# Optimization experiments

Measured on AMD Instinct MI355X. Metric: run time of the kernel, lower is better.

## Reference

```python
import jax, jax.numpy as jnp
import numpy as np

D = 2048
N = 16384
E = 8
THRESHOLD = 0.5


def setup_inputs() -> dict:
    key = jax.random.key(0)
    ks = jax.random.split(key, 6)
    x = jax.random.normal(ks[0], (N, D), dtype=jnp.float32)
    # pretrained weight + truncated SVD basis (frozen in original module)
    W_np = np.asarray(jax.random.normal(ks[1], (D, D), dtype=jnp.float32))
    U, S, Vt = np.linalg.svd(W_np, full_matrices=False)
    k = int((np.cumsum(S) < THRESHOLD * S.sum()).sum())  # energy-threshold rank
    U_k = jnp.asarray(U[:, :k])
    V_k = jnp.asarray(Vt.T[:, :k])  # torch.svd returns V, not V^T
    W = jnp.asarray(W_np)
    lambda_k = jax.random.normal(ks[2], (E, k), dtype=jnp.float32)
    v = jnp.zeros((D,), dtype=jnp.float32)
    W_g1 = jax.random.normal(ks[3], (k, 1), dtype=jnp.float32)
    W_g2 = jax.random.normal(ks[4], (1, E), dtype=jnp.float32)
    return {"x": x, "W": W, "U_k": U_k, "V_k": V_k, "lambda_k": lambda_k,
            "v": v, "W_g1": W_g1, "W_g2": W_g2}


def reference(x, W, U_k, V_k, lambda_k, v, W_g1, W_g2):
    # Routing: g = softmax((x @ U_k) @ W_g1 @ W_g2)  -> [N, E]
    xu = x @ U_k                                   # [N, k] (shared with delta path)
    g = jax.nn.softmax((xu @ W_g1) @ W_g2, axis=-1)
    # sum_i g_i * (x @ (W + U diag(lam_i) V^T))
    #   = (x@W) * sum_i g_i  +  ((x@U) * (g @ lam)) @ V^T   (low-rank factored)
    base = x @ W                                   # [N, D], computed once
    coef = g @ lambda_k                            # [N, k]
    out = base * jnp.sum(g, axis=-1, keepdims=True) + (xu * coef) @ V_k.T
    return out * (1.0 + v)
```

## Files before the change

### kernel.cpp

```cpp
#include <hip/hip_runtime.h>
#include <hip/hip_bf16.h>

#define D_DIM 2048
#define E_DIM 8

typedef __attribute__((ext_vector_type(8))) short short8;
typedef __attribute__((ext_vector_type(4))) float f32x4;

__device__ __forceinline__ unsigned short f2bf(float f) {
  union { float f; unsigned int u; } v; v.f = f;
  unsigned int u = v.u;
  u += 0x7FFFu + ((u >> 16) & 1u);
  return (unsigned short)(u >> 16);
}

__device__ __forceinline__ void async_copy16(const void* g, void* l) {
  __builtin_amdgcn_global_load_lds((const __attribute__((address_space(1))) void*)g,
                                   (__attribute__((address_space(3))) void*)l,
                                   16, 0, 0);
}

__global__ void k_transpose_bf16(const float* __restrict__ in, int in_rows, int in_cols,
                                 int in_ld, unsigned short* __restrict__ out, int out_rows) {
  __shared__ float tile[32][33];
  const int tx = threadIdx.x;
  const int ty = threadIdx.y;
  const int c = blockIdx.x * 32 + tx;
  #pragma unroll
  for (int i = 0; i < 4; ++i) {
    const int r = blockIdx.y * 32 + ty + i * 8;
    float vv = 0.0f;
    if (r < in_rows && c < in_cols) vv = in[(size_t)r * in_ld + c];
    tile[ty + i * 8][tx] = vv;
  }
  __syncthreads();
  const int oc = blockIdx.y * 32 + tx;
  #pragma unroll
  for (int i = 0; i < 4; ++i) {
    const int orow = blockIdx.x * 32 + ty + i * 8;
    if (orow < out_rows && oc < in_rows)
      out[(size_t)orow * in_rows + oc] = f2bf(tile[tx][ty + i * 8]);
  }
}

__global__ void k_pad_bf16(const float* __restrict__ in, unsigned short* __restrict__ out,
                           int rows, int cols, int cols_pad) {
  long long idx = (long long)blockIdx.x * blockDim.x + threadIdx.x;
  const long long total = (long long)rows * cols_pad;
  const long long stride = (long long)gridDim.x * blockDim.x;
  for (; idx < total; idx += stride) {
    const int r = (int)(idx / cols_pad);
    const int c = (int)(idx % cols_pad);
    out[idx] = (c < cols) ? f2bf(in[(size_t)r * cols + c]) : (unsigned short)0;
  }
}

__global__ void k_u1(const float* __restrict__ U, const float* __restrict__ Wg1,
                     float* __restrict__ u1, int D, int k) {
  const int w = threadIdx.x >> 6;
  const int lane = threadIdx.x & 63;
  const int d = blockIdx.x * 4 + w;
  if (d >= D) return;
  const float* row = U + (size_t)d * k;
  float s = 0.0f;
  for (int j = lane; j < k; j += 64) s += row[j] * Wg1[j];
  #pragma unroll
  for (int off = 32; off; off >>= 1) s += __shfl_xor(s, off);
  if (lane == 0) u1[d] = s;
}

__global__ void k_cvtgate(const float* __restrict__ x,
                          unsigned short* __restrict__ xb,
                          const float* __restrict__ u1, const float* __restrict__ Wg2,
                          float* __restrict__ g8, int Nrows) {
  const int w = threadIdx.x >> 6;
  const int lane = threadIdx.x & 63;
  const int row = blockIdx.x * 4 + w;
  if (row >= Nrows) return;
  const float* xr = x + (size_t)row * D_DIM;
  unsigned short* xo = xb + (size_t)row * D_DIM;
  float s = 0.0f;
  #pragma unroll
  for (int t = 0; t < D_DIM / 512; ++t) {
    const int base = (t * 64 + lane) * 8;
    float4 a = *(const float4*)(xr + base);
    float4 b = *(const float4*)(xr + base + 4);
    float4 ua = *(const float4*)(u1 + base);
    float4 ub = *(const float4*)(u1 + base + 4);
    s += a.x * ua.x + a.y * ua.y + a.z * ua.z + a.w * ua.w +
         b.x * ub.x + b.y * ub.y + b.z * ub.z + b.w * ub.w;
    short8 r;
    r[0] = (short)f2bf(a.x); r[1] = (short)f2bf(a.y);
    r[2] = (short)f2bf(a.z); r[3] = (short)f2bf(a.w);
    r[4] = (short)f2bf(b.x); r[5] = (short)f2bf(b.y);
    r[6] = (short)f2bf(b.z); r[7] = (short)f2bf(b.w);
    *(short8*)(xo + base) = r;
  }
  #pragma unroll
  for (int off = 32; off; off >>= 1) s += __shfl_xor(s, off);
  if (lane == 0) {
    float lg[E_DIM], mx = -INFINITY;
    #pragma unroll
    for (int e = 0; e < E_DIM; ++e) { lg[e] = s * Wg2[e]; mx = fmaxf(mx, lg[e]); }
    float Z = 0.0f;
    #pragma unroll
    for (int e = 0; e < E_DIM; ++e) { lg[e] = expf(lg[e] - mx); Z += lg[e]; }
    const float inv = 1.0f / Z;
    #pragma unroll
    for (int e = 0; e < E_DIM; ++e) g8[(size_t)row * E_DIM + e] = lg[e] * inv;
  }
}

__global__ __launch_bounds__(256, 3) void k_gemm128(
    const unsigned short* __restrict__ A, long long lda,
    const unsigned short* __restrict__ B, long long ldb,
    int Ktot,
    const float* __restrict__ g8, const float* __restrict__ lam, int k_real,
    unsigned short* __restrict__ A2, int lda2) {
  __shared__ unsigned short lds[2 * 8192];
  const int tid = threadIdx.x;
  const int lane = tid & 63;
  const int w = tid >> 6;
  const long long brow = (long long)blockIdx.x * 128;
  const long long bcol = (long long)blockIdx.y * 128;
  const int c0 = w * 2;
  const int sr0 = lane >> 2;
  const int sj  = lane & 3;
  const int l15 = lane & 15;
  const int jhi = lane >> 4;
  const int wr = (w >> 1) * 64;
  const int wc = (w & 1) * 64;

  auto stage = [&](int tt) {
    unsigned short* dstA = lds + (tt & 1) * 8192;
    #pragma unroll
    for (int c = 0; c < 2; ++c) {
      const int chunk = c0 + c;
      const int lrow = chunk * 16 + sr0;
      const int jj = sj ^ ((lrow >> 1) & 3);
      async_copy16(A + (brow + lrow) * lda + (long long)tt * 32 + jj * 8,
                   (void*)(dstA + chunk * 512));
      async_copy16(B + (bcol + lrow) * ldb + (long long)tt * 32 + jj * 8,
                   (void*)(dstA + 4096 + chunk * 512));
    }
  };

  f32x4 acc[4][4];
  #pragma unroll
  for (int m = 0; m < 4; ++m)
    #pragma unroll
    for (int n = 0; n < 4; ++n)
      #pragma unroll
      for (int j = 0; j < 4; ++j) acc[m][n][j] = 0.0f;

  const int NT = Ktot >> 5;
  stage(0);
  asm volatile("s_waitcnt vmcnt(0)" ::: "memory");
  __builtin_amdgcn_s_barrier();

  for (int t = 0; t < NT; ++t) {
    const unsigned short* Areg = lds + (t & 1) * 8192;
    const unsigned short* Breg = Areg + 4096;
    if (t + 1 < NT) stage(t + 1);
    short8 av[4], bv[4];
    #pragma unroll
    for (int m = 0; m < 4; ++m) {
      const int row = wr + m * 16 + l15;
      const int jj = jhi ^ ((row >> 1) & 3);
      av[m] = *(const short8*)(Areg + row * 32 + jj * 8);
    }
    #pragma unroll
    for (int n = 0; n < 4; ++n) {
      const int row = wc + n * 16 + l15;
      const int jj = jhi ^ ((row >> 1) & 3);
      bv[n] = *(const short8*)(Breg + row * 32 + jj * 8);
    }
    __builtin_amdgcn_s_setprio(1);
    #pragma unroll
    for (int m = 0; m < 4; ++m)
      #pragma unroll
      for (int n = 0; n < 4; ++n)
        acc[m][n] = __builtin_amdgcn_mfma_f32_16x16x32_bf16(av[m], bv[n], acc[m][n], 0, 0, 0);
    __builtin_amdgcn_s_setprio(0);
    asm volatile("s_waitcnt vmcnt(0)" ::: "memory");
    __builtin_amdgcn_s_barrier();
  }

  float lamE[E_DIM][4];
  #pragma unroll
  for (int n = 0; n < 4; ++n) {
    const long long col = bcol + wc + n * 16 + l15;
    #pragma unroll
    for (int e = 0; e < E_DIM; ++e)
      lamE[e][n] = (col < k_real) ? lam[(size_t)e * k_real + col] : 0.0f;
  }
  #pragma unroll
  for (int m = 0; m < 4; ++m) {
    float coef[4][4];
    #pragma unroll
    for (int j = 0; j < 4; ++j)
      #pragma unroll
      for (int n = 0; n < 4; ++n) coef[j][n] = 0.0f;
    #pragma unroll
    for (int j = 0; j < 4; ++j) {
      const long long row = brow + wr + m * 16 + jhi * 4 + j;
      const float* gr = g8 + row * E_DIM;
      #pragma unroll
      for (int e = 0; e < E_DIM; ++e) {
        const float ge = gr[e];
        #pragma unroll
        for (int n = 0; n < 4; ++n) coef[j][n] += ge * lamE[e][n];
      }
    }
    #pragma unroll
    for (int n = 0; n < 4; ++n) {
      const long long col = bcol + wc + n * 16 + l15;
      #pragma unroll
      for (int j = 0; j < 4; ++j) {
        const long long row = brow + wr + m * 16 + jhi * 4 + j;
        A2[row * lda2 + col] = f2bf(acc[m][n][j] * coef[j][n]);
      }
    }
  }
}

template<int EPI>
__global__ __launch_bounds__(512, 2) void k_gemm256(
    const unsigned short* __restrict__ A0, int lda0,
    const unsigned short* __restrict__ A1, int lda1,
    const unsigned short* __restrict__ B0, int ldb0,
    const unsigned short* __restrict__ B1, int ldb1,
    int ka0, int Ktot, int gridM,
    float* __restrict__ Cout, int ldc,
    const float* __restrict__ vcol) {
  __shared__ unsigned short lds[4 * 16384];
  const int tid = threadIdx.x;
  const int lane = tid & 63;
  const int w = tid >> 6;
  const int wm = w >> 2;
  const int wn = w & 3;

  int bid = blockIdx.x;
  const int cpx = gridDim.x >> 3;
  bid = (bid & 7) * cpx + (bid >> 3);
  const int bx = bid % gridM;
  const int by = bid / gridM;
  const long long brow = (long long)bx * 256;
  const long long bcol = (long long)by * 256;

  const int c0 = w * 2;
  const int sr0 = lane >> 2;
  const int sj  = lane & 3;
  const int l15 = lane & 15;
  const int jhi = lane >> 4;

  auto stage = [&](int tt) {
    const int k0 = tt * 32;
    const unsigned short* PA; long long ldA; long long kA;
    const unsigned short* PB; long long ldB; long long kB;
    if (k0 < ka0) { PA = A0; ldA = lda0; kA = k0;       PB = B0; ldB = ldb0; kB = k0; }
    else          { PA = A1; ldA = lda1; kA = k0 - ka0; PB = B1; ldB = ldb1; kB = k0 - ka0; }
    unsigned short* dst = lds + (tt & 3) * 16384;
    #pragma unroll
    for (int c = 0; c < 2; ++c) {
      const int chunk = c0 + c;
      const int lrow = chunk * 16 + sr0;
      const int jj = sj ^ ((lrow >> 1) & 3);
      async_copy16(PA + (brow + lrow) * ldA + kA + jj * 8, (void*)(dst + chunk * 512));
      async_copy16(PB + (bcol + lrow) * ldB + kB + jj * 8, (void*)(dst + 8192 + chunk * 512));
    }
  };

  auto load_frags = [&](int tt, short8* av, short8* bv) {
    const unsigned short* Areg = lds + (tt & 3) * 16384;
    const unsigned short* Breg = Areg + 8192;
    #pragma unroll
    for (int m = 0; m < 8; ++m) {
      const int row = wm * 128 + m * 16 + l15;
      const int jj = jhi ^ ((row >> 1) & 3);
      av[m] = *(const short8*)(Areg + row * 32 + jj * 8);
    }
    #pragma unroll
    for (int n = 0; n < 4; ++n) {
      const int row = wn * 64 + n * 16 + l15;
      const int jj = jhi ^ ((row >> 1) & 3);
      bv[n] = *(const short8*)(Breg + row * 32 + jj * 8);
    }
  };

  f32x4 acc[8][4];
  #pragma unroll
  for (int m = 0; m < 8; ++m)
    #pragma unroll
    for (int n = 0; n < 4; ++n)
      #pragma unroll
      for (int j = 0; j < 4; ++j) acc[m][n][j] = 0.0f;

  auto do_mfma = [&](short8* av, short8* bv) {
    __builtin_amdgcn_s_setprio(1);
    #pragma unroll
    for (int m = 0; m < 8; ++m)
      #pragma unroll
      for (int n = 0; n < 4; ++n)
        acc[m][n] = __builtin_amdgcn_mfma_f32_16x16x32_bf16(av[m], bv[n], acc[m][n], 0, 0, 0);
    __builtin_amdgcn_s_setprio(0);
  };

  const int NT = Ktot >> 5;
  stage(0); stage(1); stage(2);
  asm volatile("s_waitcnt vmcnt(4)" ::: "memory");
  __builtin_amdgcn_s_barrier();

  short8 avA[8], bvA[4], avB[8], bvB[4];
  load_frags(0, avA, bvA);

  for (int t = 0; t < NT; t += 2) {
    if (t + 3 < NT) stage(t + 3);
    load_frags(t + 1, avB, bvB);
    do_mfma(avA, bvA);
    asm volatile("s_waitcnt vmcnt(4)" ::: "memory");
    __builtin_amdgcn_s_barrier();
    if (t + 4 < NT) stage(t + 4);
    if (t + 2 < NT) load_frags(t + 2, avA, bvA);
    do_mfma(avB, bvB);
    asm volatile("s_waitcnt vmcnt(4)" ::: "memory");
    __builtin_amdgcn_s_barrier();
  }

  #pragma unroll
  for (int m = 0; m < 8; ++m) {
    #pragma unroll
    for (int n = 0; n < 4; ++n) {
      const long long col = bcol + wn * 64 + n * 16 + l15;
      float cs = 1.0f;
      if (EPI == 1) cs = 1.0f + vcol[col];
      #pragma unroll
      for (int j = 0; j < 4; ++j) {
        const long long row = brow + wm * 128 + m * 16 + jhi * 4 + j;
        Cout[row * ldc + col] = acc[m][n][j] * cs;
      }
    }
  }
}

extern "C" void kernel_launch(void* const* d_in, const int* in_sizes, int n_in,
                              void* d_out, int out_size, void* d_ws, size_t ws_size,
                              hipStream_t stream) {
  const float* x   = (const float*)d_in[0];
  const float* W   = (const float*)d_in[1];
  const float* U   = (const float*)d_in[2];
  const float* V   = (const float*)d_in[3];
  const float* lam = (const float*)d_in[4];
  const float* v   = (const float*)d_in[5];
  const float* Wg1 = (const float*)d_in[6];
  const float* Wg2 = (const float*)d_in[7];
  float* out = (float*)d_out;

  const int N = in_sizes[0] / D_DIM;
  const int k = in_sizes[2] / D_DIM;
  const int k_pad = (k + 127) & ~127;

  char* ws = (char*)d_ws;
  size_t off = 0;
  auto alloc = [&](size_t bytes) -> void* {
    void* p = ws + off;
    off += (bytes + 255) & ~(size_t)255;
    return p;
  };
  unsigned short* xb  = (unsigned short*)alloc((size_t)N * D_DIM * 2);
  unsigned short* Wt  = (unsigned short*)alloc((size_t)D_DIM * D_DIM * 2);
  unsigned short* Ukt = (unsigned short*)alloc((size_t)k_pad * D_DIM * 2);
  unsigned short* Vb  = (unsigned short*)alloc((size_t)D_DIM * k_pad * 2);
  unsigned short* A2  = (unsigned short*)alloc((size_t)N * k_pad * 2);
  float*          u1  = (float*)alloc((size_t)D_DIM * 4);
  float*          g8  = (float*)alloc((size_t)N * E_DIM * 4);
  if (off > ws_size) return;

  k_u1<<<D_DIM / 4, 256, 0, stream>>>(U, Wg1, u1, D_DIM, k);
  k_cvtgate<<<N / 4, 256, 0, stream>>>(x, xb, u1, Wg2, g8, N);
  k_transpose_bf16<<<dim3(D_DIM / 32, D_DIM / 32), dim3(32, 8), 0, stream>>>(
      W, D_DIM, D_DIM, D_DIM, Wt, D_DIM);
  k_transpose_bf16<<<dim3(k_pad / 32, D_DIM / 32), dim3(32, 8), 0, stream>>>(
      U, D_DIM, k, k, Ukt, k_pad);
  k_pad_bf16<<<512, 256, 0, stream>>>(V, Vb, D_DIM, k, k_pad);

  k_gemm128<<<dim3(N / 128, k_pad / 128), 256, 0, stream>>>(
      xb, D_DIM, Ukt, D_DIM, D_DIM, g8, lam, k, A2, k_pad);

  const int gridM = N / 256;
  const int gridN = D_DIM / 256;
  k_gemm256<1><<<gridM * gridN, 512, 0, stream>>>(
      xb, D_DIM, A2, k_pad,
      Wt, D_DIM, Vb, k_pad,
      D_DIM, D_DIM + k_pad, gridM,
      out, D_DIM, v);
}
```

Baseline: 311.1 us.

## Restructure 256x256 GEMM mainloop into K=64 double-buffered, quarter-wise staged pipeline

Replaces the four-stage K=32 LDS ring with a two-buffer K=64 layout. Each iteration is split into four MFMA quarters, and the async loads for the next tile's A and B halves are interleaved between those quarters. The LDS swizzle changes to an XOR over 8-element chunks per 64-wide row, and fragment reads are reused across sub-blocks to cut register pressure. The aim is finer overlap of global-to-LDS traffic with MFMA work. The cost is more barriers per iteration and subtle correctness risk in the buffer-reuse ordering.

```diff
diff --git a/kernel.cpp b/kernel.cpp
--- a/kernel.cpp
+++ b/kernel.cpp
@@ -233,7 +233,7 @@
     int ka0, int Ktot, int gridM,
     float* __restrict__ Cout, int ldc,
     const float* __restrict__ vcol) {
-  __shared__ unsigned short lds[4 * 16384];
+  __shared__ unsigned short lds[65536];
   const int tid = threadIdx.x;
   const int lane = tid & 63;
   const int w = tid >> 6;
@@ -248,46 +248,29 @@
   const long long brow = (long long)bx * 256;
   const long long bcol = (long long)by * 256;
 
-  const int c0 = w * 2;
-  const int sr0 = lane >> 2;
-  const int sj  = lane & 3;
   const int l15 = lane & 15;
   const int jhi = lane >> 4;
-
-  auto stage = [&](int tt) {
-    const int k0 = tt * 32;
-    const unsigned short* PA; long long ldA; long long kA;
-    const unsigned short* PB; long long ldB; long long kB;
-    if (k0 < ka0) { PA = A0; ldA = lda0; kA = k0;       PB = B0; ldB = ldb0; kB = k0; }
-    else          { PA = A1; ldA = lda1; kA = k0 - ka0; PB = B1; ldB = ldb1; kB = k0 - ka0; }
-    unsigned short* dst = lds + (tt & 3) * 16384;
-    #pragma unroll
-    for (int c = 0; c < 2; ++c) {
-      const int chunk = c0 + c;
-      const int lrow = chunk * 16 + sr0;
-      const int jj = sj ^ ((lrow >> 1) & 3);
-      async_copy16(PA + (brow + lrow) * ldA + kA + jj * 8, (void*)(dst + chunk * 512));
-      async_copy16(PB + (bcol + lrow) * ldB + kB + jj * 8, (void*)(dst + 8192 + chunk * 512));
-    }
+  const int srow0 = tid >> 3;
+  const int pcol  = ((tid & 7) ^ (srow0 & 7)) * 8;
+  const int o0 = (jhi ^ (l15 & 7)) * 8;
+  const int o1 = o0 ^ 32;
+
+  auto stage_half = [&](int tt, int op, int h) {
+    const int k0 = tt * 64;
+    const unsigned short* P; long long ld; long long kb; long long rb;
+    if (op == 0) {
+      if (k0 < ka0) { P = A0; ld = lda0; kb = k0; } else { P = A1; ld = lda1; kb = k0 - ka0; }
+      rb = brow;
+    } else {
+      if (k0 < ka0) { P = B0; ld = ldb0; kb = k0; } else { P = B1; ld = ldb1; kb = k0 - ka0; }
+      rb = bcol;
+    }
+    unsigned short* dst = lds + (tt & 1) * 32768 + op * 16384 + h * 8192 + tid * 8;
+    const unsigned short* src = P + (rb + h * 128 + srow0) * ld + kb + pcol;
+    async_copy16(src, (void*)dst);
+    async_copy16(src + 64 * ld, (void*)(dst + 4096));
   };
 
-  auto load_frags = [&](int tt, short8* av, short8* bv) {
-    const unsigned short* Areg = lds + (tt & 3) * 16384;
-    const unsigned short* Breg = Areg + 8192;
-    #pragma unroll
-    for (int m = 0; m < 8; ++m) {
-      const int row = wm * 128 + m * 16 + l15;
-      const int jj = jhi ^ ((row >> 1) & 3);
-      av[m] = *(const short8*)(Areg + row * 32 + jj * 8);
-    }
-    #pragma unroll
-    for (int n = 0; n < 4; ++n) {
-      const int row = wn * 64 + n * 16 + l15;
-      const int jj = jhi ^ ((row >> 1) & 3);
-      bv[n] = *(const short8*)(Breg + row * 32 + jj * 8);
-    }
-  };
-
   f32x4 acc[8][4];
   #pragma unroll
   for (int m = 0; m < 8; ++m)
@@ -296,34 +279,104 @@
       #pragma unroll
       for (int j = 0; j < 4; ++j) acc[m][n][j] = 0.0f;
 
-  auto do_mfma = [&](short8* av, short8* bv) {
+  const int NT = Ktot >> 6;
+
+  stage_half(0, 0, 0); stage_half(0, 0, 1);
+  stage_half(0, 1, 0); stage_half(0, 1, 1);
+  if (NT > 1) {
+    stage_half(1, 1, 0); stage_half(1, 1, 1);
+    asm volatile("s_waitcnt vmcnt(4)" ::: "memory");
+  } else {
+    asm volatile("s_waitcnt vmcnt(0)" ::: "memory");
+  }
+  __builtin_amdgcn_s_barrier();
+
+  for (int t = 0; t < NT; ++t) {
+    const unsigned short* Ab = lds + (t & 1) * 32768 + wm * 8192 + l15 * 64;
+    const unsigned short* Bb = lds + (t & 1) * 32768 + 16384 + (wn >> 1) * 8192 +
+                               (wn & 1) * 4096 + l15 * 64;
+    short8 av[8], bv0[4], bv1[4];
+
+    #pragma unroll
+    for (int m2 = 0; m2 < 4; ++m2) {
+      av[m2 * 2 + 0] = *(const short8*)(Ab + m2 * 1024 + o0);
+      av[m2 * 2 + 1] = *(const short8*)(Ab + m2 * 1024 + o1);
+    }
+    #pragma unroll
+    for (int n2 = 0; n2 < 2; ++n2) {
+      bv0[n2 * 2 + 0] = *(const short8*)(Bb + n2 * 1024 + o0);
+      bv0[n2 * 2 + 1] = *(const short8*)(Bb + n2 * 1024 + o1);
+    }
+    if (t + 1 < NT) stage_half(t + 1, 0, 0);
+    __builtin_amdgcn_s_barrier();
+    asm volatile("s_waitcnt lgkmcnt(0)" ::: "memory");
     __builtin_amdgcn_s_setprio(1);
     #pragma unroll
-    for (int m = 0; m < 8; ++m)
-      #pragma unroll
-      for (int n = 0; n < 4; ++n)
-        acc[m][n] = __builtin_amdgcn_mfma_f32_16x16x32_bf16(av[m], bv[n], acc[m][n], 0, 0, 0);
+    for (int m2 = 0; m2 < 4; ++m2)
+      #pragma unroll
+      for (int n2 = 0; n2 < 2; ++n2)
+        #pragma unroll
+        for (int k2 = 0; k2 < 2; ++k2)
+          acc[m2][n2] = __builtin_amdgcn_mfma_f32_16x16x32_bf16(
+              av[m2 * 2 + k2], bv0[n2 * 2 + k2], acc[m2][n2], 0, 0, 0);
     __builtin_amdgcn_s_setprio(0);
-  };
-
-  const int NT = Ktot >> 5;
-  stage(0); stage(1); stage(2);
-  asm volatile("s_waitcnt vmcnt(4)" ::: "memory");
-  __builtin_amdgcn_s_barrier();
-
-  short8 avA[8], bvA[4], avB[8], bvB[4];
-  load_frags(0, avA, bvA);
-
-  for (int t = 0; t < NT; t += 2) {
-    if (t + 3 < NT) stage(t + 3);
-    load_frags(t + 1, avB, bvB);
-    do_mfma(avA, bvA);
-    asm volatile("s_waitcnt vmcnt(4)" ::: "memory");
-    __builtin_amdgcn_s_barrier();
-    if (t + 4 < NT) stage(t + 4);
-    if (t + 2 < NT) load_frags(t + 2, avA, bvA);
-    do_mfma(avB, bvB);
-    asm volatile("s_waitcnt vmcnt(4)" ::: "memory");
+    __builtin_amdgcn_s_barrier();
+
+    #pragma unroll
+    for (int n2 = 0; n2 < 2; ++n2) {
+      bv1[n2 * 2 + 0] = *(const short8*)(Bb + 2048 + n2 * 1024 + o0);
+      bv1[n2 * 2 + 1] = *(const short8*)(Bb + 2048 + n2 * 1024 + o1);
+    }
+    if (t + 1 < NT) stage_half(t + 1, 0, 1);
+    __builtin_amdgcn_s_barrier();
+    asm volatile("s_waitcnt lgkmcnt(0)" ::: "memory");
+    __builtin_amdgcn_s_setprio(1);
+    #pragma unroll
+    for (int m2 = 0; m2 < 4; ++m2)
+      #pragma unroll
+      for (int n2 = 0; n2 < 2; ++n2)
+        #pragma unroll
+        for (int k2 = 0; k2 < 2; ++k2)
+          acc[m2][2 + n2] = __builtin_amdgcn_mfma_f32_16x16x32_bf16(
+              av[m2 * 2 + k2], bv1[n2 * 2 + k2], acc[m2][2 + n2], 0, 0, 0);
+    __builtin_amdgcn_s_setprio(0);
+    __builtin_amdgcn_s_barrier();
+
+    #pragma unroll
+    for (int m2 = 0; m2 < 4; ++m2) {
+      av[m2 * 2 + 0] = *(const short8*)(Ab + 4096 + m2 * 1024 + o0);
+      av[m2 * 2 + 1] = *(const short8*)(Ab + 4096 + m2 * 1024 + o1);
+    }
+    if (t + 2 < NT) stage_half(t + 2, 1, 0);
+    __builtin_amdgcn_s_barrier();
+    asm volatile("s_waitcnt lgkmcnt(0)" ::: "memory");
+    __builtin_amdgcn_s_setprio(1);
+    #pragma unroll
+    for (int m2 = 0; m2 < 4; ++m2)
+      #pragma unroll
+      for (int n2 = 0; n2 < 2; ++n2)
+        #pragma unroll
+        for (int k2 = 0; k2 < 2; ++k2)
+          acc[4 + m2][2 + n2] = __builtin_amdgcn_mfma_f32_16x16x32_bf16(
+              av[m2 * 2 + k2], bv1[n2 * 2 + k2], acc[4 + m2][2 + n2], 0, 0, 0);
+    __builtin_amdgcn_s_setprio(0);
+    __builtin_amdgcn_s_barrier();
+
+    if (t + 2 < NT) stage_half(t + 2, 1, 1);
+    __builtin_amdgcn_s_barrier();
+    asm volatile("s_waitcnt lgkmcnt(0)" ::: "memory");
+    __builtin_amdgcn_s_setprio(1);
+    #pragma unroll
+    for (int m2 = 0; m2 < 4; ++m2)
+      #pragma unroll
+      for (int n2 = 0; n2 < 2; ++n2)
+        #pragma unroll
+        for (int k2 = 0; k2 < 2; ++k2)
+          acc[4 + m2][n2] = __builtin_amdgcn_mfma_f32_16x16x32_bf16(
+              av[m2 * 2 + k2], bv0[n2 * 2 + k2], acc[4 + m2][n2], 0, 0, 0);
+    __builtin_amdgcn_s_setprio(0);
+    if (t + 2 < NT)      asm volatile("s_waitcnt vmcnt(4)" ::: "memory");
+    else if (t + 1 < NT) asm volatile("s_waitcnt vmcnt(0)" ::: "memory");
     __builtin_amdgcn_s_barrier();
   }
 
```

Result: no change. 313.2 us (+0.6%).
